# Performance work log

Measured on AMD Instinct MI355X. Metric: run time of the kernel, lower is better.

Reference implementation:

```python
import jax, jax.numpy as jnp
import numpy as np

LEAKY_SLOPE = 0.2
N_HEADS = 8
INPUT_DIM = 128
HEAD_DIM = 16  # embed_dim=128 // n_heads=8


def setup_inputs() -> dict:
    key = jax.random.key(0)
    k1, k2, k3, k4 = jax.random.split(key, 4)
    b, n = 4, 512
    h = jax.random.normal(k1, (b, n, INPUT_DIM), dtype=jnp.float32)
    mask = jnp.zeros((b, n, n), dtype=bool)  # 1 = attention not possible
    stdv_w = 1.0 / np.sqrt(HEAD_DIM)
    Wl = jax.random.uniform(k2, (N_HEADS, INPUT_DIM, HEAD_DIM), minval=-stdv_w, maxval=stdv_w, dtype=jnp.float32)
    Wr = jax.random.uniform(k3, (N_HEADS, INPUT_DIM, HEAD_DIM), minval=-stdv_w, maxval=stdv_w, dtype=jnp.float32)
    # Wak in torch is (n_heads, head_dim, 1); stdv = 1/sqrt(size(-1)) = 1
    Wak = jax.random.uniform(k4, (N_HEADS, HEAD_DIM), minval=-1.0, maxval=1.0, dtype=jnp.float32)
    return {"h": h, "mask": mask, "Wl": Wl, "Wr": Wr, "Wak": Wak}


def reference(h, mask, Wl, Wr, Wak):
    b, n, _ = h.shape
    # per-head projections: g = h @ W  -> (heads, batch, N, head_dim)
    g_l = jnp.einsum('bni,hid->hbnd', h, Wl)
    g_r = jnp.einsum('bni,hid->hbnd', h, Wr)
    # additive attention: LeakyReLU(g_l_i + g_r_j) . a  -> (heads, batch, N, N)
    e = jax.nn.leaky_relu(g_l[:, :, :, None, :] + g_r[:, :, None, :, :],
                          negative_slope=LEAKY_SLOPE)
    scores = jnp.einsum('hbijd,hd->hbij', e, Wak)
    scores = jnp.where(mask[None], -jnp.inf, scores)
    attn = jax.nn.softmax(scores, axis=-1)
    # weighted sum of g_r, then ReLU; output layout (batch, N, heads*head_dim)
    h_prime = jax.nn.relu(jnp.einsum('hbij,hbjd->bihd', attn, g_r))
    return h_prime.reshape(b, n, -1)
```

## Files before the change

kernel.cpp:

```cpp
#include <hip/hip_runtime.h>
#include <hip/hip_bf16.h>

#define B_SZ 4
#define N_SZ 512
#define IN_DIM 128
#define NH 8
#define HD 16
#define SLOPE 0.2f

typedef float v2f __attribute__((ext_vector_type(2)));

#define WS_GL 0
#define WS_GR (NH * B_SZ * N_SZ * HD)
#define WS_TOT (2 * WS_GR)

#define PM 32
#define PKC 64
#define AT_S 38
#define BT_S 68

__global__ __launch_bounds__(256) void proj_gemm(
    const float* __restrict__ hin, const float* __restrict__ Wl,
    const float* __restrict__ Wr, float* __restrict__ gl, float* __restrict__ gr)
{
    __shared__ float At[PKC * AT_S];
    __shared__ float Bs[PKC * BT_S];

    int rt = blockIdx.x >> 2;
    int ct = blockIdx.x & 3;
    int side = ct >> 1;
    int headbase = (ct & 1) * 4;
    const float* Wsrc = side ? Wr : Wl;
    int rowbase = rt * PM;

    int t = threadIdx.x;
    int ty = t >> 4;
    int tx = t & 15;

    float acc[2][4] = {{0.f,0.f,0.f,0.f},{0.f,0.f,0.f,0.f}};

    for (int kc = 0; kc < IN_DIM; kc += PKC) {
        __syncthreads();
#pragma unroll
        for (int it = 0; it < 2; ++it) {
            int task = it * 256 + t;
            int r = task >> 4, kq = task & 15;
            float4 v = *(const float4*)&hin[(size_t)(rowbase + r) * IN_DIM + kc + kq * 4];
            At[(kq * 4 + 0) * AT_S + r] = v.x;
            At[(kq * 4 + 1) * AT_S + r] = v.y;
            At[(kq * 4 + 2) * AT_S + r] = v.z;
            At[(kq * 4 + 3) * AT_S + r] = v.w;
        }
#pragma unroll
        for (int it = 0; it < 4; ++it) {
            int task = it * 256 + t;
            int k = task >> 4, cc4 = task & 15;
            int head = headbase + (cc4 >> 2);
            int dq = (cc4 & 3) * 4;
            float4 v = *(const float4*)&Wsrc[head * (IN_DIM * HD) + (kc + k) * HD + dq];
            *(float4*)&Bs[k * BT_S + cc4 * 4] = v;
        }
        __syncthreads();

#pragma unroll 16
        for (int k = 0; k < PKC; ++k) {
            float2 a = *(const float2*)&At[k * AT_S + ty * 2];
            float4 b = *(const float4*)&Bs[k * BT_S + tx * 4];
            acc[0][0] = fmaf(a.x, b.x, acc[0][0]);
            acc[0][1] = fmaf(a.x, b.y, acc[0][1]);
            acc[0][2] = fmaf(a.x, b.z, acc[0][2]);
            acc[0][3] = fmaf(a.x, b.w, acc[0][3]);
            acc[1][0] = fmaf(a.y, b.x, acc[1][0]);
            acc[1][1] = fmaf(a.y, b.y, acc[1][1]);
            acc[1][2] = fmaf(a.y, b.z, acc[1][2]);
            acc[1][3] = fmaf(a.y, b.w, acc[1][3]);
        }
    }

    int head = headbase + (tx >> 2);
    int d4 = (tx & 3) * 4;
    float* g = side ? gr : gl;
#pragma unroll
    for (int r = 0; r < 2; ++r) {
        int row = rowbase + ty * 2 + r;
        int b = row >> 9, i = row & (N_SZ - 1);
        float4 v = {acc[r][0], acc[r][1], acc[r][2], acc[r][3]};
        *(float4*)&g[((size_t)(head * B_SZ + b) * N_SZ + i) * HD + d4] = v;
    }
}

__global__ __launch_bounds__(256) void attn_wave(
    const float* __restrict__ gl, const float* __restrict__ gr,
    const float* __restrict__ Wak, const unsigned char* __restrict__ mask,
    float* __restrict__ out)
{
    int bid = blockIdx.x;
    int hb = bid >> 6;
    int head = hb >> 2, b = hb & 3;
    int t = threadIdx.x;
    int wv = t >> 6;
    int lane = t & 63;
    int jh = lane >> 1;
    int h = lane & 1;

    int pair = (bid & 63) * 4 + wv;
    int i0 = pair * 2;

    const float* grb = gr + (size_t)hb * (N_SZ * HD);
    const float* gl0 = gl + ((size_t)hb * N_SZ + i0) * HD;
    const float* ap = Wak + head * HD;

    float a[8], w0[8], w1[8];
    {
        float4 a0 = *(const float4*)(ap + h * 8);
        float4 a1 = *(const float4*)(ap + h * 8 + 4);
        float4 u0 = *(const float4*)(gl0 + h * 8);
        float4 u1 = *(const float4*)(gl0 + h * 8 + 4);
        float4 v0 = *(const float4*)(gl0 + HD + h * 8);
        float4 v1 = *(const float4*)(gl0 + HD + h * 8 + 4);
        a[0]=a0.x; a[1]=a0.y; a[2]=a0.z; a[3]=a0.w;
        a[4]=a1.x; a[5]=a1.y; a[6]=a1.z; a[7]=a1.w;
        w0[0]=u0.x; w0[1]=u0.y; w0[2]=u0.z; w0[3]=u0.w;
        w0[4]=u1.x; w0[5]=u1.y; w0[6]=u1.z; w0[7]=u1.w;
        w1[0]=v0.x; w1[1]=v0.y; w1[2]=v0.z; w1[3]=v0.w;
        w1[4]=v1.x; w1[5]=v1.y; w1[6]=v1.z; w1[7]=v1.w;
    }

    const unsigned char* m0p = mask + ((size_t)(b * N_SZ + i0)) * N_SZ;
    const unsigned char* m1p = m0p + N_SZ;

    float o0[8], o1[8];
#pragma unroll
    for (int k = 0; k < 8; ++k) { o0[k] = 0.f; o1[k] = 0.f; }
    float l0 = 0.f, l1 = 0.f;

#pragma unroll 4
    for (int it = 0; it < N_SZ / 32; ++it) {
        int j = it * 32 + jh;
        const float* src = grb + it * 512 + lane * 8;
        float4 ga = *(const float4*)src;
        float4 gb = *(const float4*)(src + 4);
        float g[8] = {ga.x, ga.y, ga.z, ga.w, gb.x, gb.y, gb.z, gb.w};

        float u = 0.f, s0p = 0.f, s1p = 0.f;
#pragma unroll
        for (int k = 0; k < 8; ++k) {
            u = fmaf(a[k], g[k], u);
            s0p = fmaf(a[k], fabsf(w0[k] + g[k]), s0p);
            s1p = fmaf(a[k], fabsf(w1[k] + g[k]), s1p);
        }
        float u06 = 0.6f * u;
        float s0 = fmaf(0.4f, s0p, u06);
        float s1 = fmaf(0.4f, s1p, u06);
        s0 += __shfl_xor(s0, 1, 64);
        s1 += __shfl_xor(s1, 1, 64);

        unsigned char mm0 = m0p[j];
        unsigned char mm1 = m1p[j];
        s0 = mm0 ? -1e30f : fminf(s0, 80.f);
        s1 = mm1 ? -1e30f : fminf(s1, 80.f);

        float p0 = __expf(s0);
        float p1 = __expf(s1);
        l0 += p0; l1 += p1;
#pragma unroll
        for (int k = 0; k < 8; ++k) {
            o0[k] = fmaf(p0, g[k], o0[k]);
            o1[k] = fmaf(p1, g[k], o1[k]);
        }
    }

#pragma unroll
    for (int off = 2; off < 64; off <<= 1) {
        l0 += __shfl_xor(l0, off, 64);
        l1 += __shfl_xor(l1, off, 64);
#pragma unroll
        for (int k = 0; k < 8; ++k) {
            o0[k] += __shfl_xor(o0[k], off, 64);
            o1[k] += __shfl_xor(o1[k], off, 64);
        }
    }

    if (lane < 4) {
        int r = lane >> 1;
        float li = r ? l1 : l0;
        float inv = 1.f / li;
        const float* oo = r ? o1 : o0;
        float res[8];
#pragma unroll
        for (int k = 0; k < 8; ++k)
            res[k] = fmaxf(oo[k] * inv, 0.f);
        float* op = out + ((size_t)(b * N_SZ + i0 + r)) * (NH * HD)
                        + head * HD + (lane & 1) * 8;
        *(float4*)op = *(float4*)res;
        *(float4*)(op + 4) = *(float4*)(res + 4);
    }
}

__global__ __launch_bounds__(512) void gatv2_fused(
    const float* __restrict__ hin, const unsigned char* __restrict__ mask,
    const float* __restrict__ Wl, const float* __restrict__ Wr,
    const float* __restrict__ Wak, float* __restrict__ out)
{
    __shared__ float wrs[IN_DIM * HD];
    __shared__ float hsh[32][IN_DIM + 1];
    __shared__ float grs[N_SZ * 18];
    __shared__ float gls[32][HD];

    int bid = blockIdx.x;
    int itile = bid & 15;
    int hb = bid >> 4;
    int head = hb >> 2, b = hb & 3;
    int t = threadIdx.x;

    int jl = t >> 4;
    int d  = t & 15;

    for (int idx = t; idx < IN_DIM * HD; idx += 512)
        wrs[idx] = Wr[head * IN_DIM * HD + idx];

    const float* hb_base = hin + (size_t)b * N_SZ * IN_DIM;
    const float* wlcol = Wl + head * IN_DIM * HD + d;

    for (int c = 0; c < N_SZ / 32; ++c) {
        __syncthreads();
        const float* hc = hb_base + (size_t)c * 32 * IN_DIM;
        for (int idx = t; idx < 32 * IN_DIM; idx += 512)
            hsh[idx >> 7][idx & 127] = hc[idx];
        __syncthreads();

        float acc = 0.f;
#pragma unroll 16
        for (int k = 0; k < IN_DIM; ++k)
            acc = fmaf(hsh[jl][k], wrs[k * HD + d], acc);
        grs[(c * 32 + jl) * 18 + d] = acc;

        if (c == itile) {
            float accl = 0.f;
#pragma unroll 16
            for (int k = 0; k < IN_DIM; ++k)
                accl = fmaf(hsh[jl][k], wlcol[k * HD], accl);
            gls[jl][d] = accl;
        }
    }
    __syncthreads();

    int il = jl, jt = d;
    int i = itile * 32 + il;

    float glv[HD], avv[HD];
#pragma unroll
    for (int dd = 0; dd < HD; ++dd) glv[dd] = gls[il][dd];
    const float* ap = Wak + head * HD;
#pragma unroll
    for (int dd = 0; dd < HD; ++dd) avv[dd] = ap[dd];

    const unsigned char* mrow = mask + ((size_t)(b * N_SZ + i)) * N_SZ;

    float m = -1e30f, l = 0.f;
    float o[HD];
#pragma unroll
    for (int dd = 0; dd < HD; ++dd) o[dd] = 0.f;

    for (int jj = 0; jj < N_SZ / 16; ++jj) {
        int j = jj * 16 + jt;
        const float* r = &grs[j * 18];
        float gj[HD];
#pragma unroll
        for (int e = 0; e < HD / 2; ++e) {
            float2 v = *(const float2*)(r + 2 * e);
            gj[2 * e] = v.x; gj[2 * e + 1] = v.y;
        }

        float s = 0.f;
#pragma unroll
        for (int dd = 0; dd < HD; ++dd) {
            float x = glv[dd] + gj[dd];
            float lr = fmaxf(x, SLOPE * x);
            s = fmaf(avv[dd], lr, s);
        }
        if (mrow[j]) s = -1e30f;

        float mn = fmaxf(m, s);
        float cc = __expf(m - mn);
        float p = __expf(s - mn);
        l = fmaf(l, cc, p);
#pragma unroll
        for (int dd = 0; dd < HD; ++dd)
            o[dd] = fmaf(o[dd], cc, p * gj[dd]);
        m = mn;
    }

#pragma unroll
    for (int off = 1; off < 16; off <<= 1) {
        float mo = __shfl_xor(m, off, 64);
        float lo = __shfl_xor(l, off, 64);
        float mn = fmaxf(m, mo);
        float c1 = __expf(m - mn), c2 = __expf(mo - mn);
        l = l * c1 + lo * c2;
#pragma unroll
        for (int dd = 0; dd < HD; ++dd)
            o[dd] = o[dd] * c1 + __shfl_xor(o[dd], off, 64) * c2;
        m = mn;
    }

    if (jt == 0) {
        float inv = 1.f / l;
        float res[HD];
#pragma unroll
        for (int dd = 0; dd < HD; ++dd)
            res[dd] = fmaxf(o[dd] * inv, 0.f);
        float* op = out + ((size_t)(b * N_SZ + i)) * (NH * HD) + head * HD;
#pragma unroll
        for (int e = 0; e < HD / 4; ++e)
            *(float4*)(op + 4 * e) = *(float4*)(res + 4 * e);
    }
}

extern "C" void kernel_launch(void* const* d_in, const int* in_sizes, int n_in,
                              void* d_out, int out_size, void* d_ws, size_t ws_size,
                              hipStream_t stream) {
    const float* hin = (const float*)d_in[0];
    const unsigned char* mask = (const unsigned char*)d_in[1];
    const float* Wl = (const float*)d_in[2];
    const float* Wr = (const float*)d_in[3];
    const float* Wak = (const float*)d_in[4];
    float* out = (float*)d_out;
    (void)in_sizes; (void)n_in; (void)out_size;

    const size_t need = (size_t)WS_TOT * sizeof(float);

    if (ws_size >= need && d_ws != nullptr) {
        float* ws = (float*)d_ws;
        float* gl = ws + WS_GL;
        float* gr = ws + WS_GR;
        proj_gemm<<<(B_SZ * N_SZ / PM) * 4, 256, 0, stream>>>(hin, Wl, Wr, gl, gr);
        attn_wave<<<NH * B_SZ * 64, 256, 0, stream>>>(gl, gr, Wak, mask, out);
    } else {
        gatv2_fused<<<NH * B_SZ * (N_SZ / 32), 512, 0, stream>>>(
            hin, mask, Wl, Wr, Wak, out);
    }
}
```

Baseline: 89.64 us.

## Process four query rows per wave with packed float2 math in attention kernel

Each wave in the attention kernel now handles four query rows instead of two, so every g_r tile load and the shared a·g term are reused across more rows, and the grid is halved. The inner arithmetic is rewritten with 2-wide float vectors so the compiler can emit packed FP32 adds and FMAs. In exchange, each thread holds more registers (four rows of accumulators and g_l values), which may lower occupancy, and halving the block count reduces parallelism across the GPU.

After: 97.13 us. 1.08x slower.

```diff
diff --git a/kernel.cpp b/kernel.cpp
--- a/kernel.cpp
+++ b/kernel.cpp
@@ -95,103 +95,120 @@
     float* __restrict__ out)
 {
     int bid = blockIdx.x;
-    int hb = bid >> 6;
+    int hb = bid >> 5;
     int head = hb >> 2, b = hb & 3;
     int t = threadIdx.x;
     int wv = t >> 6;
     int lane = t & 63;
     int jh = lane >> 1;
     int h = lane & 1;
-
-    int pair = (bid & 63) * 4 + wv;
-    int i0 = pair * 2;
+    int i0 = ((bid & 31) * 4 + wv) * 4;
 
     const float* grb = gr + (size_t)hb * (N_SZ * HD);
     const float* gl0 = gl + ((size_t)hb * N_SZ + i0) * HD;
     const float* ap = Wak + head * HD;
 
-    float a[8], w0[8], w1[8];
+    float a[8];
     {
         float4 a0 = *(const float4*)(ap + h * 8);
         float4 a1 = *(const float4*)(ap + h * 8 + 4);
-        float4 u0 = *(const float4*)(gl0 + h * 8);
-        float4 u1 = *(const float4*)(gl0 + h * 8 + 4);
-        float4 v0 = *(const float4*)(gl0 + HD + h * 8);
-        float4 v1 = *(const float4*)(gl0 + HD + h * 8 + 4);
         a[0]=a0.x; a[1]=a0.y; a[2]=a0.z; a[3]=a0.w;
         a[4]=a1.x; a[5]=a1.y; a[6]=a1.z; a[7]=a1.w;
-        w0[0]=u0.x; w0[1]=u0.y; w0[2]=u0.z; w0[3]=u0.w;
-        w0[4]=u1.x; w0[5]=u1.y; w0[6]=u1.z; w0[7]=u1.w;
-        w1[0]=v0.x; w1[1]=v0.y; w1[2]=v0.z; w1[3]=v0.w;
-        w1[4]=v1.x; w1[5]=v1.y; w1[6]=v1.z; w1[7]=v1.w;
-    }
-
-    const unsigned char* m0p = mask + ((size_t)(b * N_SZ + i0)) * N_SZ;
-    const unsigned char* m1p = m0p + N_SZ;
-
-    float o0[8], o1[8];
-#pragma unroll
-    for (int k = 0; k < 8; ++k) { o0[k] = 0.f; o1[k] = 0.f; }
-    float l0 = 0.f, l1 = 0.f;
-
-#pragma unroll 4
+    }
+
+    v2f w[4][4], o[4][4];
+#pragma unroll
+    for (int r = 0; r < 4; ++r) {
+        float4 u0 = *(const float4*)(gl0 + r * HD + h * 8);
+        float4 u1 = *(const float4*)(gl0 + r * HD + h * 8 + 4);
+        w[r][0] = (v2f){u0.x, u0.y}; w[r][1] = (v2f){u0.z, u0.w};
+        w[r][2] = (v2f){u1.x, u1.y}; w[r][3] = (v2f){u1.z, u1.w};
+#pragma unroll
+        for (int e = 0; e < 4; ++e) o[r][e] = (v2f){0.f, 0.f};
+    }
+
+    const unsigned char* mrow = mask + ((size_t)(b * N_SZ + i0)) * N_SZ;
+    float l[4] = {0.f, 0.f, 0.f, 0.f};
+
+#pragma unroll 2
     for (int it = 0; it < N_SZ / 32; ++it) {
         int j = it * 32 + jh;
         const float* src = grb + it * 512 + lane * 8;
         float4 ga = *(const float4*)src;
         float4 gb = *(const float4*)(src + 4);
-        float g[8] = {ga.x, ga.y, ga.z, ga.w, gb.x, gb.y, gb.z, gb.w};
-
-        float u = 0.f, s0p = 0.f, s1p = 0.f;
-#pragma unroll
-        for (int k = 0; k < 8; ++k) {
-            u = fmaf(a[k], g[k], u);
-            s0p = fmaf(a[k], fabsf(w0[k] + g[k]), s0p);
-            s1p = fmaf(a[k], fabsf(w1[k] + g[k]), s1p);
+        unsigned char mm0 = mrow[j];
+        unsigned char mm1 = mrow[N_SZ + j];
+        unsigned char mm2 = mrow[2 * N_SZ + j];
+        unsigned char mm3 = mrow[3 * N_SZ + j];
+        v2f g[4] = {(v2f){ga.x, ga.y}, (v2f){ga.z, ga.w},
+                    (v2f){gb.x, gb.y}, (v2f){gb.z, gb.w}};
+
+        float u = 0.f;
+#pragma unroll
+        for (int e = 0; e < 4; ++e) {
+            u = fmaf(a[2 * e],     g[e].x, u);
+            u = fmaf(a[2 * e + 1], g[e].y, u);
         }
         float u06 = 0.6f * u;
-        float s0 = fmaf(0.4f, s0p, u06);
-        float s1 = fmaf(0.4f, s1p, u06);
-        s0 += __shfl_xor(s0, 1, 64);
-        s1 += __shfl_xor(s1, 1, 64);
-
-        unsigned char mm0 = m0p[j];
-        unsigned char mm1 = m1p[j];
-        s0 = mm0 ? -1e30f : fminf(s0, 80.f);
-        s1 = mm1 ? -1e30f : fminf(s1, 80.f);
-
-        float p0 = __expf(s0);
-        float p1 = __expf(s1);
-        l0 += p0; l1 += p1;
-#pragma unroll
-        for (int k = 0; k < 8; ++k) {
-            o0[k] = fmaf(p0, g[k], o0[k]);
-            o1[k] = fmaf(p1, g[k], o1[k]);
+
+        float s[4];
+#pragma unroll
+        for (int r = 0; r < 4; ++r) {
+            float sp0 = 0.f, sp1 = 0.f;
+#pragma unroll
+            for (int e = 0; e < 4; ++e) {
+                v2f x = w[r][e] + g[e];
+                sp0 = fmaf(a[2 * e],     fabsf(x.x), sp0);
+                sp1 = fmaf(a[2 * e + 1], fabsf(x.y), sp1);
+            }
+            s[r] = fmaf(0.4f, sp0 + sp1, u06);
+        }
+#pragma unroll
+        for (int r = 0; r < 4; ++r)
+            s[r] += __shfl_xor(s[r], 1, 64);
+
+        s[0] = mm0 ? -1e30f : fminf(s[0], 80.f);
+        s[1] = mm1 ? -1e30f : fminf(s[1], 80.f);
+        s[2] = mm2 ? -1e30f : fminf(s[2], 80.f);
+        s[3] = mm3 ? -1e30f : fminf(s[3], 80.f);
+
+#pragma unroll
+        for (int r = 0; r < 4; ++r) {
+            float p = __expf(s[r]);
+            l[r] += p;
+            v2f pv = (v2f){p, p};
+#pragma unroll
+            for (int e = 0; e < 4; ++e)
+                o[r][e] += pv * g[e];
         }
     }
 
 #pragma unroll
     for (int off = 2; off < 64; off <<= 1) {
-        l0 += __shfl_xor(l0, off, 64);
-        l1 += __shfl_xor(l1, off, 64);
-#pragma unroll
-        for (int k = 0; k < 8; ++k) {
-            o0[k] += __shfl_xor(o0[k], off, 64);
-            o1[k] += __shfl_xor(o1[k], off, 64);
-        }
-    }
-
-    if (lane < 4) {
+#pragma unroll
+        for (int r = 0; r < 4; ++r) {
+            l[r] += __shfl_xor(l[r], off, 64);
+#pragma unroll
+            for (int e = 0; e < 4; ++e) {
+                v2f q;
+                q.x = __shfl_xor(o[r][e].x, off, 64);
+                q.y = __shfl_xor(o[r][e].y, off, 64);
+                o[r][e] += q;
+            }
+        }
+    }
+
+    if (lane < 8) {
         int r = lane >> 1;
-        float li = r ? l1 : l0;
-        float inv = 1.f / li;
-        const float* oo = r ? o1 : o0;
+        float inv = 1.f / l[r];
         float res[8];
 #pragma unroll
-        for (int k = 0; k < 8; ++k)
-            res[k] = fmaxf(oo[k] * inv, 0.f);
+        for (int e = 0; e < 4; ++e) {
+            res[2 * e]     = fmaxf(o[r][e].x * inv, 0.f);
+            res[2 * e + 1] = fmaxf(o[r][e].y * inv, 0.f);
+        }
         float* op = out + ((size_t)(b * N_SZ + i0 + r)) * (NH * HD)
-                        + head * HD + (lane & 1) * 8;
+                        + head * HD + h * 8;
         *(float4*)op = *(float4*)res;
         *(float4*)(op + 4) = *(float4*)(res + 4);
     }
@@ -335,7 +352,7 @@
         float* gl = ws + WS_GL;
         float* gr = ws + WS_GR;
         proj_gemm<<<(B_SZ * N_SZ / PM) * 4, 256, 0, stream>>>(hin, Wl, Wr, gl, gr);
-        attn_wave<<<NH * B_SZ * 64, 256, 0, stream>>>(gl, gr, Wak, mask, out);
+        attn_wave<<<NH * B_SZ * 32, 256, 0, stream>>>(gl, gr, Wak, mask, out);
     } else {
         gatv2_fused<<<NH * B_SZ * (N_SZ / 32), 512, 0, stream>>>(
             hin, mask, Wl, Wr, Wak, out);
```
